# Performance work log

Hardware: AMD Instinct MI355X
Metric: run time of the kernel (lower is better)

Reference implementation:

```python
import jax, jax.numpy as jnp
import numpy as np

NUM_HEADS = 16
DIM_HEADS = 64
DIM_INPUT = 1024
DIM = NUM_HEADS * DIM_HEADS  # 1024


def setup_inputs() -> dict:
    key = jax.random.key(0)
    ks = jax.random.split(key, 8)
    B, S = 2, 2048
    inputs = jax.random.normal(ks[0], (B, S, DIM_INPUT), dtype=jnp.float32)
    attention_mask = jnp.zeros((B, 1, 1, S), dtype=jnp.float32)
    s = 1.0 / np.sqrt(DIM_INPUT)
    Wq = jax.random.normal(ks[1], (DIM_INPUT, DIM), dtype=jnp.float32) * s
    bq = jnp.zeros((DIM,), dtype=jnp.float32)
    Wk = jax.random.normal(ks[2], (DIM_INPUT, DIM), dtype=jnp.float32) * s
    bk = jnp.zeros((DIM,), dtype=jnp.float32)
    Wv = jax.random.normal(ks[3], (DIM_INPUT, DIM), dtype=jnp.float32) * s
    bv = jnp.zeros((DIM,), dtype=jnp.float32)
    return {"inputs": inputs, "attention_mask": attention_mask,
            "Wq": Wq, "bq": bq, "Wk": Wk, "bk": bk, "Wv": Wv, "bv": bv}


def _split_heads(x):
    # [B, S, H*dh] -> [B, H, S, dh]
    B, S, _ = x.shape
    return x.reshape(B, S, NUM_HEADS, DIM_HEADS).transpose(0, 2, 1, 3)


def reference(inputs, attention_mask, Wq, bq, Wk, bk, Wv, bv):
    q = _split_heads(inputs @ Wq + bq)  # [B,H,S,dh]
    k = _split_heads(inputs @ Wk + bk)
    v = _split_heads(inputs @ Wv + bv)
    scores = jnp.einsum('bhsd,bhtd->bhst', q, k) / np.sqrt(DIM_HEADS).astype(np.float32)
    scores = scores + attention_mask  # broadcast additive mask
    probs = jax.nn.softmax(scores, axis=-1)  # dropout is identity in eval
    ctx = jnp.einsum('bhst,bhtd->bhsd', probs, v)  # [B,H,S,dh]
    B, H, S, dh = ctx.shape
    return ctx.transpose(0, 2, 1, 3).reshape(B, S, H * dh)
```

## Files before the change

kernel.cpp:

```cpp
#include <hip/hip_runtime.h>


typedef __attribute__((ext_vector_type(4))) float f32x4;
typedef __attribute__((ext_vector_type(16))) float f32x16;
typedef __attribute__((ext_vector_type(8))) __bf16 bf16x8;

#define DEV static __device__ __forceinline__

constexpr int S_ = 2048;
constexpr int H_ = 16;
constexpr int DH_ = 64;
constexpr int DIN_ = 1024;
constexpr int M_ = 2 * S_;
constexpr int N3_ = 3 * 1024;
constexpr int K_ = DIN_;
constexpr float LOG2E = 1.44269504088896340736f;

DEV unsigned short f2bf(float f) {
  unsigned u = __builtin_bit_cast(unsigned, f);
  u += 0x7fffu + ((u >> 16) & 1u);
  return (unsigned short)(u >> 16);
}

DEV unsigned cvt_pk(float lo, float hi) {
  unsigned d;
  asm("v_cvt_pk_bf16_f32 %0, %1, %2" : "=v"(d) : "v"(lo), "v"(hi));
  return d;
}

DEV void gload_lds16(const void* g, void* l) {
  __builtin_amdgcn_global_load_lds(
      (const __attribute__((address_space(1))) unsigned int*)g,
      (__attribute__((address_space(3))) unsigned int*)l, 16, 0, 0);
}

DEV int kswz(int row, int colb) { return row * 128 + (colb ^ ((row & 7) << 4)); }

__global__ __launch_bounds__(256) void convert_x(const float* __restrict__ X,
                                                 unsigned short* __restrict__ Xbf) {
  int idx = (blockIdx.x * 256 + threadIdx.x) * 8;
  float4 a = *(const float4*)(X + idx);
  float4 b = *(const float4*)(X + idx + 4);
  unsigned short r[8];
  r[0] = f2bf(a.x); r[1] = f2bf(a.y); r[2] = f2bf(a.z); r[3] = f2bf(a.w);
  r[4] = f2bf(b.x); r[5] = f2bf(b.y); r[6] = f2bf(b.z); r[7] = f2bf(b.w);
  *(uint4*)(Xbf + idx) = *(uint4*)r;
}

__global__ __launch_bounds__(256) void transpose_w(const float* __restrict__ Wq,
                                                   const float* __restrict__ Wk,
                                                   const float* __restrict__ Wv,
                                                   unsigned short* __restrict__ Wt) {
  __shared__ float tile[32][33];
  int z = blockIdx.z;
  const float* W = (z == 0) ? Wq : (z == 1) ? Wk : Wv;
  int n0 = blockIdx.x * 32, k0 = blockIdx.y * 32;
  int tx = threadIdx.x, ty = threadIdx.y;
  for (int i = 0; i < 4; ++i)
    tile[ty + i * 8][tx] = W[(size_t)(k0 + ty + i * 8) * 1024 + n0 + tx];
  __syncthreads();
  for (int i = 0; i < 4; ++i)
    Wt[(size_t)(z * 1024 + n0 + ty + i * 8) * 1024 + k0 + tx] =
        f2bf(tile[tx][ty + i * 8]);
}

__global__ __launch_bounds__(256, 2) void qkv_gemm(
    const unsigned short* __restrict__ Xbf, const unsigned short* __restrict__ Wt,
    const float* __restrict__ bq, const float* __restrict__ bk,
    const float* __restrict__ bv, unsigned short* __restrict__ Qw,
    unsigned short* __restrict__ Kw, unsigned short* __restrict__ Vt) {
  __shared__ unsigned short Abuf[128 * 64];
  __shared__ unsigned short Bbuf[128 * 64];
  int tid = threadIdx.x;
  int w = tid >> 6, l = tid & 63;
  int row16 = l & 15, kg = l >> 4;
  int mBase = blockIdx.y * 128, nBase = blockIdx.x * 128;
  int wm = w >> 1, wn = w & 1;

  f32x4 acc[4][4] = {};

  const int grow = l >> 3;
  const int gcol = ((l & 7) ^ grow) * 8;

  for (int kt = 0; kt < K_ / 64; ++kt) {
    int k0 = kt * 64;
    __syncthreads();
#pragma unroll
    for (int j = 0; j < 4; ++j) {
      int c1k = w * 4 + j;
      int r = c1k * 8 + grow;
      gload_lds16(Xbf + (size_t)(mBase + r) * K_ + k0 + gcol,
                  (char*)Abuf + c1k * 1024);
      gload_lds16(Wt + (size_t)(nBase + r) * K_ + k0 + gcol,
                  (char*)Bbuf + c1k * 1024);
    }
    __syncthreads();
#pragma unroll
    for (int kk = 0; kk < 2; ++kk) {
      bf16x8 af[4], bfr[4];
#pragma unroll
      for (int m = 0; m < 4; ++m)
        af[m] = *(const bf16x8*)((const char*)Abuf +
                 kswz(wm * 64 + m * 16 + row16, kk * 64 + kg * 16));
#pragma unroll
      for (int n = 0; n < 4; ++n)
        bfr[n] = *(const bf16x8*)((const char*)Bbuf +
                  kswz(wn * 64 + n * 16 + row16, kk * 64 + kg * 16));
#pragma unroll
      for (int m = 0; m < 4; ++m)
#pragma unroll
        for (int n = 0; n < 4; ++n)
          acc[m][n] = __builtin_amdgcn_mfma_f32_16x16x32_bf16(af[m], bfr[n],
                                                              acc[m][n], 0, 0, 0);
    }
  }

#pragma unroll
  for (int n = 0; n < 4; ++n) {
    int gn = nBase + wn * 64 + n * 16 + row16;
    int which = gn >> 10;
    int nn = gn & 1023;
    float bias = (which == 0 ? bq : which == 1 ? bk : bv)[nn];
    unsigned short* dst = (which == 0) ? Qw : (which == 1) ? Kw : Vt;
    float scl = (which == 0) ? 0.125f * LOG2E : 1.0f;
    int hh = nn >> 6, dd = nn & 63;
#pragma unroll
    for (int m = 0; m < 4; ++m) {
      int gm0 = mBase + wm * 64 + m * 16 + kg * 4;
#pragma unroll
      for (int j = 0; j < 4; ++j) {
        int gm = gm0 + j;
        int bb = gm >> 11, ss = gm & 2047;
        float v = (acc[m][n][j] + bias) * scl;
        size_t idx;
        if (which == 2)
          idx = ((size_t)(bb * H_ + hh) * DH_ + dd) * S_ + ss;
        else
          idx = ((size_t)(bb * H_ + hh) * S_ + ss) * DH_ + dd;
        dst[idx] = f2bf(v);
      }
    }
  }
}

__global__ __launch_bounds__(512, 4) void attn_fwd(
    const unsigned short* __restrict__ Qw, const unsigned short* __restrict__ Kw,
    const unsigned short* __restrict__ Vt, const float* __restrict__ mask,
    float* __restrict__ out) {
  __shared__ __align__(16) char LDS[73728];

  const int tid = threadIdx.x;
  const int w = tid >> 6, l = tid & 63;
  const int qg = w >> 1, thalf = w & 1;
  const int lq = l & 31;
  const int h = l >> 5;
  const int wgid = blockIdx.x;
  const int xcd = wgid & 7, ixd = wgid >> 3;
  const int bh = xcd + 8 * (ixd >> 4);
  const int qt = ixd & 15;
  const int b = bh >> 4, hh = bh & 15;
  const int q0 = qt * 128 + qg * 32;

  const unsigned short* Kb = Kw + (size_t)bh * S_ * DH_;
  const unsigned short* Vb = Vt + (size_t)bh * DH_ * S_;

  {
    float4 mv = *(const float4*)(mask + (size_t)b * S_ + tid * 4);
    mv.x *= LOG2E; mv.y *= LOG2E; mv.z *= LOG2E; mv.w *= LOG2E;
    *(float4*)(LDS + tid * 16) = mv;
  }

  bf16x8 qf[4];
  {
    const unsigned short* qrow = Qw + ((size_t)bh * S_ + q0 + lq) * DH_;
#pragma unroll
    for (int kk = 0; kk < 4; ++kk)
      qf[kk] = *(const bf16x8*)(qrow + kk * 16 + h * 8);
  }

  int rb[4];
#pragma unroll
  for (int kk = 0; kk < 4; ++kk)
    rb[kk] = 8192 + thalf * 8192 + lq * 128 + ((kk * 32 + h * 16) ^ ((lq & 7) << 4));
  const int srow = tid >> 3;
  const int tc8 = (tid & 7) * 8;
  const int wb = 8192 + srow * 128 + (((tid & 7) * 16) ^ ((srow & 7) << 4));
  const int mb = thalf * 256 + h * 16;

  bf16x8 kr[2], vr[2];
#pragma unroll
  for (int j = 0; j < 2; ++j) {
    kr[j] = *(const bf16x8*)(Kb + (size_t)(j * 64 + srow) * DH_ + tc8);
    vr[j] = *(const bf16x8*)(Vb + (size_t)srow * S_ + j * 64 + tc8);
  }
#pragma unroll
  for (int j = 0; j < 2; ++j) {
    *(bf16x8*)(LDS + wb + j * 8192) = kr[j];
    *(bf16x8*)(LDS + wb + 32768 + j * 8192) = vr[j];
  }
#pragma unroll
  for (int j = 0; j < 2; ++j) {
    kr[j] = *(const bf16x8*)(Kb + (size_t)(128 + j * 64 + srow) * DH_ + tc8);
    vr[j] = *(const bf16x8*)(Vb + (size_t)srow * S_ + 128 + j * 64 + tc8);
  }
  __syncthreads();

  float l_run = 0.f;
  f32x16 O0 = {}, O1 = {};

  auto body = [&](int p, int cur) __attribute__((always_inline)) {
    if (p < 15) {
#pragma unroll
      for (int j = 0; j < 2; ++j) {
        *(bf16x8*)(LDS + wb + j * 8192 + (cur ^ 1) * 16384) = kr[j];
        *(bf16x8*)(LDS + wb + 32768 + j * 8192 + (cur ^ 1) * 16384) = vr[j];
      }
      if (p < 14) {
        const int tn = (p + 2) * 128;
#pragma unroll
        for (int j = 0; j < 2; ++j) {
          kr[j] = *(const bf16x8*)(Kb + (size_t)(tn + j * 64 + srow) * DH_ + tc8);
          vr[j] = *(const bf16x8*)(Vb + (size_t)srow * S_ + tn + j * 64 + tc8);
        }
      }
    }

    const int mo = mb + p * 512;
    f32x16 p0, p1;
#pragma unroll
    for (int r2 = 0; r2 < 4; ++r2) {
      f32x4 a = *(const f32x4*)(LDS + mo + r2 * 32);
      f32x4 bq4 = *(const f32x4*)(LDS + mo + 128 + r2 * 32);
#pragma unroll
      for (int c = 0; c < 4; ++c) { p0[4 * r2 + c] = a[c]; p1[4 * r2 + c] = bq4[c]; }
    }

    __builtin_amdgcn_s_setprio(1);
#pragma unroll
    for (int kk = 0; kk < 4; ++kk) {
      bf16x8 kf0 = *(const bf16x8*)(LDS + rb[kk] + cur * 16384);
      bf16x8 kf1 = *(const bf16x8*)(LDS + rb[kk] + 4096 + cur * 16384);
      p0 = __builtin_amdgcn_mfma_f32_32x32x16_bf16(kf0, qf[kk], p0, 0, 0, 0);
      p1 = __builtin_amdgcn_mfma_f32_32x32x16_bf16(kf1, qf[kk], p1, 0, 0, 0);
    }
    __builtin_amdgcn_s_setprio(0);

#pragma unroll
    for (int i = 0; i < 16; ++i) {
      p0[i] = __builtin_amdgcn_exp2f(p0[i]);
      p1[i] = __builtin_amdgcn_exp2f(p1[i]);
    }

    float s8[8];
#pragma unroll
    for (int i = 0; i < 8; ++i)
      s8[i] = (p0[i] + p0[i + 8]) + (p1[i] + p1[i + 8]);
    float rs = ((s8[0] + s8[1]) + (s8[2] + s8[3])) +
               ((s8[4] + s8[5]) + (s8[6] + s8[7]));
    rs += __shfl_xor(rs, 32, 64);
    l_run += rs;

    unsigned w0[8], w1[8];
#pragma unroll
    for (int r2 = 0; r2 < 4; ++r2) {
      w0[2 * r2]     = cvt_pk(p0[4 * r2 + 0], p0[4 * r2 + 1]);
      w0[2 * r2 + 1] = cvt_pk(p0[4 * r2 + 2], p0[4 * r2 + 3]);
      w1[2 * r2]     = cvt_pk(p1[4 * r2 + 0], p1[4 * r2 + 1]);
      w1[2 * r2 + 1] = cvt_pk(p1[4 * r2 + 2], p1[4 * r2 + 3]);
    }

    __builtin_amdgcn_s_setprio(1);
#pragma unroll
    for (int s = 0; s < 4; ++s) {
      const unsigned* W = (s < 2) ? w0 : w1;
      const int base = (s & 1) * 4;
      unsigned send0 = h ? W[base + 0] : W[base + 2];
      unsigned send1 = h ? W[base + 1] : W[base + 3];
      unsigned c0 = (unsigned)__shfl_xor((int)send0, 32, 64);
      unsigned c1 = (unsigned)__shfl_xor((int)send1, 32, 64);
      uint4 fw;
      fw.x = h ? c0 : W[base + 0];
      fw.y = h ? c1 : W[base + 1];
      fw.z = h ? W[base + 2] : c0;
      fw.w = h ? W[base + 3] : c1;
      bf16x8 pf = __builtin_bit_cast(bf16x8, fw);
      bf16x8 vf0 = *(const bf16x8*)(LDS + rb[s] + 32768 + cur * 16384);
      O0 = __builtin_amdgcn_mfma_f32_32x32x16_bf16(vf0, pf, O0, 0, 0, 0);
      bf16x8 vf1 = *(const bf16x8*)(LDS + rb[s] + 36864 + cur * 16384);
      O1 = __builtin_amdgcn_mfma_f32_32x32x16_bf16(vf1, pf, O1, 0, 0, 0);
    }
    __builtin_amdgcn_s_setprio(0);

    __syncthreads();
  };

#pragma unroll 1
  for (int pp = 0; pp < 8; ++pp) {
    body(2 * pp, 0);
    body(2 * pp + 1, 1);
  }

  char* Osc = LDS + 8192;
  float* Mp = (float*)LDS;
  const int sbase = qg * 8192 + l * 128;
  const int sx = (l & 7) << 4;
  if (thalf == 1) {
#pragma unroll
    for (int i = 0; i < 4; ++i) {
      f32x4 v;
#pragma unroll
      for (int c = 0; c < 4; ++c) v[c] = O0[i * 4 + c];
      *(f32x4*)(Osc + sbase + ((i * 16) ^ sx)) = v;
    }
#pragma unroll
    for (int i = 0; i < 4; ++i) {
      f32x4 v;
#pragma unroll
      for (int c = 0; c < 4; ++c) v[c] = O1[i * 4 + c];
      *(f32x4*)(Osc + sbase + (((i + 4) * 16) ^ sx)) = v;
    }
    Mp[qg * 64 + l] = l_run;
  }
  __syncthreads();
  if (thalf == 0) {
#pragma unroll
    for (int i = 0; i < 4; ++i) {
      f32x4 v = *(const f32x4*)(Osc + sbase + ((i * 16) ^ sx));
#pragma unroll
      for (int c = 0; c < 4; ++c) O0[i * 4 + c] += v[c];
    }
#pragma unroll
    for (int i = 0; i < 4; ++i) {
      f32x4 v = *(const f32x4*)(Osc + sbase + (((i + 4) * 16) ^ sx));
#pragma unroll
      for (int c = 0; c < 4; ++c) O1[i * 4 + c] += v[c];
    }
    l_run += Mp[qg * 64 + l];

    float inv = 1.0f / l_run;
    float* orow = out + ((size_t)b * S_ + q0 + lq) * 1024 + hh * 64;
#pragma unroll
    for (int r2 = 0; r2 < 4; ++r2) {
      f32x4 v0, v1;
#pragma unroll
      for (int c = 0; c < 4; ++c) {
        v0[c] = O0[4 * r2 + c] * inv;
        v1[c] = O1[4 * r2 + c] * inv;
      }
      *(f32x4*)&orow[r2 * 8 + h * 4] = v0;
      *(f32x4*)&orow[32 + r2 * 8 + h * 4] = v1;
    }
  }
}

extern "C" void kernel_launch(void* const* d_in, const int* in_sizes, int n_in,
                              void* d_out, int out_size, void* d_ws, size_t ws_size,
                              hipStream_t stream) {
  const float* X = (const float*)d_in[0];
  const float* mask = (const float*)d_in[1];
  const float* Wq = (const float*)d_in[2];
  const float* bq = (const float*)d_in[3];
  const float* Wk = (const float*)d_in[4];
  const float* bk = (const float*)d_in[5];
  const float* Wv = (const float*)d_in[6];
  const float* bv = (const float*)d_in[7];
  float* out = (float*)d_out;

  char* ws = (char*)d_ws;
  unsigned short* Xbf = (unsigned short*)ws;
  unsigned short* Wt  = (unsigned short*)(ws + (size_t)(8 << 20));
  unsigned short* Qw  = (unsigned short*)(ws + (size_t)(14 << 20));
  unsigned short* Kw  = (unsigned short*)(ws + (size_t)(22 << 20));
  unsigned short* Vt  = (unsigned short*)(ws + (size_t)(30 << 20));

  convert_x<<<dim3(M_ * K_ / (256 * 8)), dim3(256), 0, stream>>>(X, Xbf);
  transpose_w<<<dim3(32, 32, 3), dim3(32, 8), 0, stream>>>(Wq, Wk, Wv, Wt);
  qkv_gemm<<<dim3(N3_ / 128, M_ / 128), dim3(256), 0, stream>>>(
      Xbf, Wt, bq, bk, bv, Qw, Kw, Vt);
  attn_fwd<<<dim3(512), dim3(512), 0, stream>>>(Qw, Kw, Vt, mask, out);
}
```

Before: 94.80 us.

## Double query rows per wave and stage K/V via direct global-to-LDS loads

Each attention wave now processes two 32-row query tiles, so every K/V fragment read from LDS is reused twice. The block shrinks to 256 threads. Register staging of K/V is replaced by direct global-to-LDS loads, and the QKV GEMM writes K and V in a pre-swizzled layout that matches the LDS bank-conflict-avoiding pattern. Register pressure rises with the four accumulators, and occupancy changes, in exchange for fewer LDS reads and no VGPR round trip for staging.

```diff
diff --git a/kernel.cpp b/kernel.cpp
--- a/kernel.cpp
+++ b/kernel.cpp
@@ -133,17 +133,21 @@
         int bb = gm >> 11, ss = gm & 2047;
         float v = (acc[m][n][j] + bias) * scl;
         size_t idx;
-        if (which == 2)
-          idx = ((size_t)(bb * H_ + hh) * DH_ + dd) * S_ + ss;
-        else
+        if (which == 2) {
+          int cs = (ss & ~63) | ((ss & 63) ^ ((dd & 7) << 3));
+          idx = ((size_t)(bb * H_ + hh) * DH_ + dd) * S_ + cs;
+        } else if (which == 1) {
+          idx = ((size_t)(bb * H_ + hh) * S_ + ss) * DH_ + (dd ^ ((ss & 7) << 3));
+        } else {
           idx = ((size_t)(bb * H_ + hh) * S_ + ss) * DH_ + dd;
+        }
         dst[idx] = f2bf(v);
       }
     }
   }
 }
 
-__global__ __launch_bounds__(512, 4) void attn_fwd(
+__global__ __launch_bounds__(256, 2) void attn_fwd(
     const unsigned short* __restrict__ Qw, const unsigned short* __restrict__ Kw,
     const unsigned short* __restrict__ Vt, const float* __restrict__ mask,
     float* __restrict__ out) {
@@ -152,87 +156,82 @@
   const int tid = threadIdx.x;
   const int w = tid >> 6, l = tid & 63;
   const int qg = w >> 1, thalf = w & 1;
-  const int lq = l & 31;
-  const int h = l >> 5;
+  const int lq = l & 31, h = l >> 5;
   const int wgid = blockIdx.x;
   const int xcd = wgid & 7, ixd = wgid >> 3;
   const int bh = xcd + 8 * (ixd >> 4);
   const int qt = ixd & 15;
   const int b = bh >> 4, hh = bh & 15;
-  const int q0 = qt * 128 + qg * 32;
-
-  const unsigned short* Kb = Kw + (size_t)bh * S_ * DH_;
-  const unsigned short* Vb = Vt + (size_t)bh * DH_ * S_;
+  const int q0 = qt * 128 + qg * 64;
+
+  const char* KbB = (const char*)(Kw + (size_t)bh * S_ * DH_);
+  const char* VbB = (const char*)(Vt + (size_t)bh * DH_ * S_);
 
   {
-    float4 mv = *(const float4*)(mask + (size_t)b * S_ + tid * 4);
-    mv.x *= LOG2E; mv.y *= LOG2E; mv.z *= LOG2E; mv.w *= LOG2E;
-    *(float4*)(LDS + tid * 16) = mv;
-  }
-
-  bf16x8 qf[4];
+    const float* mrow = mask + (size_t)b * S_ + tid * 8;
+    float4 m0 = *(const float4*)mrow;
+    float4 m1 = *(const float4*)(mrow + 4);
+    m0.x *= LOG2E; m0.y *= LOG2E; m0.z *= LOG2E; m0.w *= LOG2E;
+    m1.x *= LOG2E; m1.y *= LOG2E; m1.z *= LOG2E; m1.w *= LOG2E;
+    *(float4*)(LDS + tid * 32) = m0;
+    *(float4*)(LDS + tid * 32 + 16) = m1;
+  }
+
+  bf16x8 qfA[4], qfB[4];
   {
-    const unsigned short* qrow = Qw + ((size_t)bh * S_ + q0 + lq) * DH_;
-#pragma unroll
-    for (int kk = 0; kk < 4; ++kk)
-      qf[kk] = *(const bf16x8*)(qrow + kk * 16 + h * 8);
+    const unsigned short* qa = Qw + ((size_t)bh * S_ + q0 + lq) * DH_;
+    const unsigned short* qb = qa + 32 * DH_;
+#pragma unroll
+    for (int kk = 0; kk < 4; ++kk) {
+      qfA[kk] = *(const bf16x8*)(qa + kk * 16 + h * 8);
+      qfB[kk] = *(const bf16x8*)(qb + kk * 16 + h * 8);
+    }
   }
 
   int rb[4];
 #pragma unroll
   for (int kk = 0; kk < 4; ++kk)
-    rb[kk] = 8192 + thalf * 8192 + lq * 128 + ((kk * 32 + h * 16) ^ ((lq & 7) << 4));
-  const int srow = tid >> 3;
-  const int tc8 = (tid & 7) * 8;
-  const int wb = 8192 + srow * 128 + (((tid & 7) * 16) ^ ((srow & 7) << 4));
-  const int mb = thalf * 256 + h * 16;
-
-  bf16x8 kr[2], vr[2];
-#pragma unroll
-  for (int j = 0; j < 2; ++j) {
-    kr[j] = *(const bf16x8*)(Kb + (size_t)(j * 64 + srow) * DH_ + tc8);
-    vr[j] = *(const bf16x8*)(Vb + (size_t)srow * S_ + j * 64 + tc8);
-  }
-#pragma unroll
-  for (int j = 0; j < 2; ++j) {
-    *(bf16x8*)(LDS + wb + j * 8192) = kr[j];
-    *(bf16x8*)(LDS + wb + 32768 + j * 8192) = vr[j];
-  }
-#pragma unroll
-  for (int j = 0; j < 2; ++j) {
-    kr[j] = *(const bf16x8*)(Kb + (size_t)(128 + j * 64 + srow) * DH_ + tc8);
-    vr[j] = *(const bf16x8*)(Vb + (size_t)srow * S_ + 128 + j * 64 + tc8);
-  }
+    rb[kk] = 8192 + thalf * 8192 + lq * 128 +
+             ((kk * 32 + h * 16) ^ ((lq & 7) << 4));
+
+  int voff[4];
+#pragma unroll
+  for (int i = 0; i < 4; ++i) {
+    int Lb = (w * 4 + i) * 1024 + l * 16;
+    voff[i] = ((Lb >> 7) & 63) * (S_ * 2) + (Lb >> 13) * 128 + (Lb & 127);
+  }
+
+  auto stage = [&](int pair, int buf) __attribute__((always_inline)) {
+#pragma unroll
+    for (int i = 0; i < 4; ++i) {
+      const int c = w * 4 + i;
+      gload_lds16(KbB + (size_t)pair * 16384 + c * 1024 + l * 16,
+                  LDS + 8192 + buf * 16384 + c * 1024);
+      gload_lds16(VbB + (size_t)pair * 256 + voff[i],
+                  LDS + 40960 + buf * 16384 + c * 1024);
+    }
+  };
+
+  stage(0, 0);
   __syncthreads();
 
-  float l_run = 0.f;
-  f32x16 O0 = {}, O1 = {};
+  float lA = 0.f, lB = 0.f;
+  f32x16 OA0 = {}, OA1 = {}, OB0 = {}, OB1 = {};
 
   auto body = [&](int p, int cur) __attribute__((always_inline)) {
-    if (p < 15) {
-#pragma unroll
-      for (int j = 0; j < 2; ++j) {
-        *(bf16x8*)(LDS + wb + j * 8192 + (cur ^ 1) * 16384) = kr[j];
-        *(bf16x8*)(LDS + wb + 32768 + j * 8192 + (cur ^ 1) * 16384) = vr[j];
-      }
-      if (p < 14) {
-        const int tn = (p + 2) * 128;
-#pragma unroll
-        for (int j = 0; j < 2; ++j) {
-          kr[j] = *(const bf16x8*)(Kb + (size_t)(tn + j * 64 + srow) * DH_ + tc8);
-          vr[j] = *(const bf16x8*)(Vb + (size_t)srow * S_ + tn + j * 64 + tc8);
-        }
-      }
-    }
-
-    const int mo = mb + p * 512;
-    f32x16 p0, p1;
+    if (p < 15) stage(p + 1, cur ^ 1);
+
+    const int mo = thalf * 256 + h * 16 + p * 512;
+    f32x16 pA0, pA1, pB0, pB1;
 #pragma unroll
     for (int r2 = 0; r2 < 4; ++r2) {
       f32x4 a = *(const f32x4*)(LDS + mo + r2 * 32);
-      f32x4 bq4 = *(const f32x4*)(LDS + mo + 128 + r2 * 32);
-#pragma unroll
-      for (int c = 0; c < 4; ++c) { p0[4 * r2 + c] = a[c]; p1[4 * r2 + c] = bq4[c]; }
+      f32x4 b4 = *(const f32x4*)(LDS + mo + 128 + r2 * 32);
+#pragma unroll
+      for (int c = 0; c < 4; ++c) {
+        pA0[4 * r2 + c] = a[c];  pB0[4 * r2 + c] = a[c];
+        pA1[4 * r2 + c] = b4[c]; pB1[4 * r2 + c] = b4[c];
+      }
     }
 
     __builtin_amdgcn_s_setprio(1);
@@ -240,54 +239,82 @@
     for (int kk = 0; kk < 4; ++kk) {
       bf16x8 kf0 = *(const bf16x8*)(LDS + rb[kk] + cur * 16384);
       bf16x8 kf1 = *(const bf16x8*)(LDS + rb[kk] + 4096 + cur * 16384);
-      p0 = __builtin_amdgcn_mfma_f32_32x32x16_bf16(kf0, qf[kk], p0, 0, 0, 0);
-      p1 = __builtin_amdgcn_mfma_f32_32x32x16_bf16(kf1, qf[kk], p1, 0, 0, 0);
+      pA0 = __builtin_amdgcn_mfma_f32_32x32x16_bf16(kf0, qfA[kk], pA0, 0, 0, 0);
+      pB0 = __builtin_amdgcn_mfma_f32_32x32x16_bf16(kf0, qfB[kk], pB0, 0, 0, 0);
+      pA1 = __builtin_amdgcn_mfma_f32_32x32x16_bf16(kf1, qfA[kk], pA1, 0, 0, 0);
+      pB1 = __builtin_amdgcn_mfma_f32_32x32x16_bf16(kf1, qfB[kk], pB1, 0, 0, 0);
     }
     __builtin_amdgcn_s_setprio(0);
 
 #pragma unroll
     for (int i = 0; i < 16; ++i) {
-      p0[i] = __builtin_amdgcn_exp2f(p0[i]);
-      p1[i] = __builtin_amdgcn_exp2f(p1[i]);
-    }
-
-    float s8[8];
-#pragma unroll
-    for (int i = 0; i < 8; ++i)
-      s8[i] = (p0[i] + p0[i + 8]) + (p1[i] + p1[i + 8]);
-    float rs = ((s8[0] + s8[1]) + (s8[2] + s8[3])) +
-               ((s8[4] + s8[5]) + (s8[6] + s8[7]));
-    rs += __shfl_xor(rs, 32, 64);
-    l_run += rs;
-
-    unsigned w0[8], w1[8];
+      pA0[i] = __builtin_amdgcn_exp2f(pA0[i]);
+      pA1[i] = __builtin_amdgcn_exp2f(pA1[i]);
+      pB0[i] = __builtin_amdgcn_exp2f(pB0[i]);
+      pB1[i] = __builtin_amdgcn_exp2f(pB1[i]);
+    }
+
+    {
+      float sA[8], sB[8];
+#pragma unroll
+      for (int i = 0; i < 8; ++i) {
+        sA[i] = (pA0[i] + pA0[i + 8]) + (pA1[i] + pA1[i + 8]);
+        sB[i] = (pB0[i] + pB0[i + 8]) + (pB1[i] + pB1[i + 8]);
+      }
+      float rsA = ((sA[0] + sA[1]) + (sA[2] + sA[3])) +
+                  ((sA[4] + sA[5]) + (sA[6] + sA[7]));
+      float rsB = ((sB[0] + sB[1]) + (sB[2] + sB[3])) +
+                  ((sB[4] + sB[5]) + (sB[6] + sB[7]));
+      rsA += __shfl_xor(rsA, 32, 64);
+      rsB += __shfl_xor(rsB, 32, 64);
+      lA += rsA;
+      lB += rsB;
+    }
+
+    unsigned wA0[8], wA1[8], wB0[8], wB1[8];
 #pragma unroll
     for (int r2 = 0; r2 < 4; ++r2) {
-      w0[2 * r2]     = cvt_pk(p0[4 * r2 + 0], p0[4 * r2 + 1]);
-      w0[2 * r2 + 1] = cvt_pk(p0[4 * r2 + 2], p0[4 * r2 + 3]);
-      w1[2 * r2]     = cvt_pk(p1[4 * r2 + 0], p1[4 * r2 + 1]);
-      w1[2 * r2 + 1] = cvt_pk(p1[4 * r2 + 2], p1[4 * r2 + 3]);
+      wA0[2 * r2]     = cvt_pk(pA0[4 * r2 + 0], pA0[4 * r2 + 1]);
+      wA0[2 * r2 + 1] = cvt_pk(pA0[4 * r2 + 2], pA0[4 * r2 + 3]);
+      wA1[2 * r2]     = cvt_pk(pA1[4 * r2 + 0], pA1[4 * r2 + 1]);
+      wA1[2 * r2 + 1] = cvt_pk(pA1[4 * r2 + 2], pA1[4 * r2 + 3]);
+      wB0[2 * r2]     = cvt_pk(pB0[4 * r2 + 0], pB0[4 * r2 + 1]);
+      wB0[2 * r2 + 1] = cvt_pk(pB0[4 * r2 + 2], pB0[4 * r2 + 3]);
+      wB1[2 * r2]     = cvt_pk(pB1[4 * r2 + 0], pB1[4 * r2 + 1]);
+      wB1[2 * r2 + 1] = cvt_pk(pB1[4 * r2 + 2], pB1[4 * r2 + 3]);
     }
 
     __builtin_amdgcn_s_setprio(1);
 #pragma unroll
     for (int s = 0; s < 4; ++s) {
-      const unsigned* W = (s < 2) ? w0 : w1;
+      const unsigned* WA = (s < 2) ? wA0 : wA1;
+      const unsigned* WB = (s < 2) ? wB0 : wB1;
       const int base = (s & 1) * 4;
-      unsigned send0 = h ? W[base + 0] : W[base + 2];
-      unsigned send1 = h ? W[base + 1] : W[base + 3];
-      unsigned c0 = (unsigned)__shfl_xor((int)send0, 32, 64);
-      unsigned c1 = (unsigned)__shfl_xor((int)send1, 32, 64);
-      uint4 fw;
-      fw.x = h ? c0 : W[base + 0];
-      fw.y = h ? c1 : W[base + 1];
-      fw.z = h ? W[base + 2] : c0;
-      fw.w = h ? W[base + 3] : c1;
-      bf16x8 pf = __builtin_bit_cast(bf16x8, fw);
+      unsigned sA0 = h ? WA[base + 0] : WA[base + 2];
+      unsigned sA1 = h ? WA[base + 1] : WA[base + 3];
+      unsigned sB0 = h ? WB[base + 0] : WB[base + 2];
+      unsigned sB1 = h ? WB[base + 1] : WB[base + 3];
+      unsigned cA0 = (unsigned)__shfl_xor((int)sA0, 32, 64);
+      unsigned cA1 = (unsigned)__shfl_xor((int)sA1, 32, 64);
+      unsigned cB0 = (unsigned)__shfl_xor((int)sB0, 32, 64);
+      unsigned cB1 = (unsigned)__shfl_xor((int)sB1, 32, 64);
+      uint4 fA, fB;
+      fA.x = h ? cA0 : WA[base + 0];
+      fA.y = h ? cA1 : WA[base + 1];
+      fA.z = h ? WA[base + 2] : cA0;
+      fA.w = h ? WA[base + 3] : cA1;
+      fB.x = h ? cB0 : WB[base + 0];
+      fB.y = h ? cB1 : WB[base + 1];
+      fB.z = h ? WB[base + 2] : cB0;
+      fB.w = h ? WB[base + 3] : cB1;
+      bf16x8 pfA = __builtin_bit_cast(bf16x8, fA);
+      bf16x8 pfB = __builtin_bit_cast(bf16x8, fB);
       bf16x8 vf0 = *(const bf16x8*)(LDS + rb[s] + 32768 + cur * 16384);
-      O0 = __builtin_amdgcn_mfma_f32_32x32x16_bf16(vf0, pf, O0, 0, 0, 0);
       bf16x8 vf1 = *(const bf16x8*)(LDS + rb[s] + 36864 + cur * 16384);
-      O1 = __builtin_amdgcn_mfma_f32_32x32x16_bf16(vf1, pf, O1, 0, 0, 0);
+      OA0 = __builtin_amdgcn_mfma_f32_32x32x16_bf16(vf0, pfA, OA0, 0, 0, 0);
+      OB0 = __builtin_amdgcn_mfma_f32_32x32x16_bf16(vf0, pfB, OB0, 0, 0, 0);
+      OA1 = __builtin_amdgcn_mfma_f32_32x32x16_bf16(vf1, pfA, OA1, 0, 0, 0);
+      OB1 = __builtin_amdgcn_mfma_f32_32x32x16_bf16(vf1, pfB, OB1, 0, 0, 0);
     }
     __builtin_amdgcn_s_setprio(0);
 
@@ -302,53 +329,53 @@
 
   char* Osc = LDS + 8192;
   float* Mp = (float*)LDS;
-  const int sbase = qg * 8192 + l * 128;
-  const int sx = (l & 7) << 4;
+  const int sbase = (qg * 64 + l) * 256;
+  const int sx = l & 15;
   if (thalf == 1) {
-#pragma unroll
-    for (int i = 0; i < 4; ++i) {
-      f32x4 v;
-#pragma unroll
-      for (int c = 0; c < 4; ++c) v[c] = O0[i * 4 + c];
-      *(f32x4*)(Osc + sbase + ((i * 16) ^ sx)) = v;
-    }
-#pragma unroll
-    for (int i = 0; i < 4; ++i) {
-      f32x4 v;
-#pragma unroll
-      for (int c = 0; c < 4; ++c) v[c] = O1[i * 4 + c];
-      *(f32x4*)(Osc + sbase + (((i + 4) * 16) ^ sx)) = v;
-    }
-    Mp[qg * 64 + l] = l_run;
+    const f32x16* Os[4] = {&OA0, &OA1, &OB0, &OB1};
+#pragma unroll
+    for (int r = 0; r < 4; ++r)
+#pragma unroll
+      for (int i = 0; i < 4; ++i) {
+        f32x4 v;
+#pragma unroll
+        for (int c = 0; c < 4; ++c) v[c] = (*Os[r])[i * 4 + c];
+        *(f32x4*)(Osc + sbase + (((r * 4 + i) ^ sx) << 4)) = v;
+      }
+    Mp[qg * 64 + l] = lA;
+    Mp[128 + qg * 64 + l] = lB;
   }
   __syncthreads();
   if (thalf == 0) {
-#pragma unroll
-    for (int i = 0; i < 4; ++i) {
-      f32x4 v = *(const f32x4*)(Osc + sbase + ((i * 16) ^ sx));
-#pragma unroll
-      for (int c = 0; c < 4; ++c) O0[i * 4 + c] += v[c];
-    }
-#pragma unroll
-    for (int i = 0; i < 4; ++i) {
-      f32x4 v = *(const f32x4*)(Osc + sbase + (((i + 4) * 16) ^ sx));
-#pragma unroll
-      for (int c = 0; c < 4; ++c) O1[i * 4 + c] += v[c];
-    }
-    l_run += Mp[qg * 64 + l];
-
-    float inv = 1.0f / l_run;
-    float* orow = out + ((size_t)b * S_ + q0 + lq) * 1024 + hh * 64;
+    f32x16* Os[4] = {&OA0, &OA1, &OB0, &OB1};
+#pragma unroll
+    for (int r = 0; r < 4; ++r)
+#pragma unroll
+      for (int i = 0; i < 4; ++i) {
+        f32x4 v = *(const f32x4*)(Osc + sbase + (((r * 4 + i) ^ sx) << 4));
+#pragma unroll
+        for (int c = 0; c < 4; ++c) (*Os[r])[i * 4 + c] += v[c];
+      }
+    lA += Mp[qg * 64 + l];
+    lB += Mp[128 + qg * 64 + l];
+
+    float invA = 1.0f / lA, invB = 1.0f / lB;
+    float* orA = out + ((size_t)b * S_ + q0 + lq) * 1024 + hh * 64;
+    float* orB = out + ((size_t)b * S_ + q0 + 32 + lq) * 1024 + hh * 64;
 #pragma unroll
     for (int r2 = 0; r2 < 4; ++r2) {
-      f32x4 v0, v1;
+      f32x4 a0, a1, b0, b1;
 #pragma unroll
       for (int c = 0; c < 4; ++c) {
-        v0[c] = O0[4 * r2 + c] * inv;
-        v1[c] = O1[4 * r2 + c] * inv;
-      }
-      *(f32x4*)&orow[r2 * 8 + h * 4] = v0;
-      *(f32x4*)&orow[32 + r2 * 8 + h * 4] = v1;
+        a0[c] = OA0[4 * r2 + c] * invA;
+        a1[c] = OA1[4 * r2 + c] * invA;
+        b0[c] = OB0[4 * r2 + c] * invB;
+        b1[c] = OB1[4 * r2 + c] * invB;
+      }
+      *(f32x4*)&orA[r2 * 8 + h * 4] = a0;
+      *(f32x4*)&orA[32 + r2 * 8 + h * 4] = a1;
+      *(f32x4*)&orB[r2 * 8 + h * 4] = b0;
+      *(f32x4*)&orB[32 + r2 * 8 + h * 4] = b1;
     }
   }
 }
@@ -377,5 +404,5 @@
   transpose_w<<<dim3(32, 32, 3), dim3(32, 8), 0, stream>>>(Wq, Wk, Wv, Wt);
   qkv_gemm<<<dim3(N3_ / 128, M_ / 128), dim3(256), 0, stream>>>(
       Xbf, Wt, bq, bk, bv, Qw, Kw, Vt);
-  attn_fwd<<<dim3(512), dim3(512), 0, stream>>>(Qw, Kw, Vt, mask, out);
-}
+  attn_fwd<<<dim3(512), dim3(256), 0, stream>>>(Qw, Kw, Vt, mask, out);
+}
```

Result: no change. 95.31 us (+0.5%).
